# Optimization experiments

Hardware: AMD Instinct MI355X
Metric: run time of the kernel (lower is better)

The kernel has to match this reference:

```python
import jax, jax.numpy as jnp
import numpy as np

N = 100000
E = 1200000
D = 64  # g_dim == h2_dim, heads=1


def setup_inputs() -> dict:
    key = jax.random.key(0)
    ks = jax.random.split(key, 12)
    s = 1.0 / np.sqrt(D)
    node_features = jax.random.normal(ks[0], (N, D), dtype=jnp.float32)
    edge_index = jax.random.randint(ks[1], (2, E), 0, N, dtype=jnp.int64)
    edge_type = jax.random.randint(ks[2], (E,), 0, 4, dtype=jnp.int64)
    Wq = jax.random.uniform(ks[3], (D, D), jnp.float32, -s, s)
    bq = jax.random.uniform(ks[4], (D,), jnp.float32, -s, s)
    Wk = jax.random.uniform(ks[5], (D, D), jnp.float32, -s, s)
    bk = jax.random.uniform(ks[6], (D,), jnp.float32, -s, s)
    Wv = jax.random.uniform(ks[7], (D, D), jnp.float32, -s, s)
    bv = jax.random.uniform(ks[8], (D,), jnp.float32, -s, s)
    Wskip = jax.random.uniform(ks[9], (D, D), jnp.float32, -s, s)
    bskip = jax.random.uniform(ks[10], (D,), jnp.float32, -s, s)
    return dict(node_features=node_features, edge_index=edge_index,
                edge_type=edge_type, Wq=Wq, bq=bq, Wk=Wk, bk=bk,
                Wv=Wv, bv=bv, Wskip=Wskip, bskip=bskip)


def _transformer_conv(x, edge_index, Wq, bq, Wk, bk, Wv, bv, Wskip, bskip):
    src, dst = edge_index[0], edge_index[1]
    q = x @ Wq + bq          # [N, D] queries (for targets)
    k = x @ Wk + bk          # [N, D] keys (for sources)
    v = x @ Wv + bv          # [N, D] values (for sources)
    scale = 1.0 / jnp.sqrt(jnp.asarray(D, x.dtype))
    # per-edge attention logits: (q_dst . k_src) / sqrt(D)   [E]
    logits = jnp.sum(q[dst] * k[src], axis=-1) * scale
    # segment softmax over incoming edges of each destination node
    seg_max = jax.ops.segment_max(logits, dst, num_segments=N)
    seg_max = jnp.where(jnp.isfinite(seg_max), seg_max, 0.0)
    ex = jnp.exp(logits - seg_max[dst])
    seg_sum = jax.ops.segment_sum(ex, dst, num_segments=N)
    alpha = ex / (seg_sum[dst] + 1e-16)                      # [E]
    # attention-weighted scatter-aggregate of source values
    out = jax.ops.segment_sum(alpha[:, None] * v[src], dst, num_segments=N)
    # root/skip connection
    return out + x @ Wskip + bskip


def reference(node_features, edge_index, edge_type, Wq, bq, Wk, bk, Wv, bv, Wskip, bskip):
    # edge_type is accepted but unused, matching the original forward.
    return _transformer_conv(node_features, edge_index, Wq, bq, Wk, bk, Wv, bv, Wskip, bskip)
```

## Files before the change

kernel.cpp:

```cpp
#include <hip/hip_runtime.h>
#include <hip/hip_fp16.h>

#define D 64
#define BSH 9
#define SPLIT_CH 4096
#define NH 512
#define QSCALE 0.18033688f

typedef _Float16 f16x2 __attribute__((ext_vector_type(2)));
typedef _Float16 f16x8 __attribute__((ext_vector_type(8)));
typedef float f32x4 __attribute__((ext_vector_type(4)));

__device__ __forceinline__ float fdot2f(f16x2 a, f16x2 b, float c) {
#if __has_builtin(__builtin_amdgcn_fdot2)
    return __builtin_amdgcn_fdot2(a, b, c, false);
#else
    return fmaf((float)a.x, (float)b.x, fmaf((float)a.y, (float)b.y, c));
#endif
}

__device__ __forceinline__ f16x2 shxor_h2(f16x2 v, int m) {
    int i = __builtin_bit_cast(int, v);
    i = __shfl_xor(i, m);
    return __builtin_bit_cast(f16x2, i);
}

__device__ __forceinline__ unsigned packh2(float a, float b) {
    __half2 h = __floats2half2_rn(a, b);
    return __builtin_bit_cast(unsigned, h);
}

__global__ __launch_bounds__(256) void k_prep(
    const float* __restrict__ Wq, const float* __restrict__ Wk,
    const float* __restrict__ Wv, const float* __restrict__ Wsk,
    const float* __restrict__ bq, const float* __restrict__ bk,
    const float* __restrict__ bv, const float* __restrict__ bsk,
    const int* __restrict__ ei, unsigned* __restrict__ wpk,
    float* __restrict__ ball, int* __restrict__ ghist, int e_cnt)
{
    const int t = threadIdx.x;
    if (blockIdx.x < 32) {
        const int u    = blockIdx.x * 256 + t;
        const int i2   = u & 3;
        const int lane = (u >> 2) & 63;
        const int ks   = (u >> 8) & 1;
        const int mt   = u >> 9;
        const int ncol = mt * 16 + (lane & 15);
        const int k0   = ks * 32 + ((lane >> 4) << 3) + (i2 << 1);
        const float* W; int c; float sc = 1.f;
        if      (ncol <  64) { W = Wq;  c = ncol;       sc = QSCALE; }
        else if (ncol < 128) { W = Wk;  c = ncol - 64;  }
        else if (ncol < 192) { W = Wv;  c = ncol - 128; }
        else                 { W = Wsk; c = ncol - 192; }
        wpk[u] = packh2(W[k0 * 64 + c] * sc, W[(k0 + 1) * 64 + c] * sc);
    } else if (blockIdx.x == 32) {
        float b;
        if      (t <  64) b = bq[t] * QSCALE;
        else if (t < 128) b = bk[t - 64];
        else if (t < 192) b = bv[t - 128];
        else              b = bsk[t - 192];
        ball[t] = b;
    } else {
        __shared__ int h[256];
        h[t] = 0;
        __syncthreads();
        const int hb    = blockIdx.x - 33;
        const int chunk = (e_cnt + NH - 1) / NH;
        const int c0    = hb * chunk;
        const int c1    = min(c0 + chunk, e_cnt);
        for (int i = c0 + t; i < c1; i += 256)
            atomicAdd(&h[ei[e_cnt + i] >> BSH], 1);
        __syncthreads();
        if (h[t]) atomicAdd(&ghist[t], h[t]);
    }
}

__global__ __launch_bounds__(256) void k_linsplit(
    const float* __restrict__ x, const unsigned* __restrict__ wpk,
    const float* __restrict__ ball, const int* __restrict__ ei,
    const int* __restrict__ ghist, int* __restrict__ gcur0,
    unsigned* __restrict__ qh, unsigned* __restrict__ kvh,
    float* __restrict__ out, unsigned* __restrict__ epack,
    int n, int e_cnt, int NLIN)
{
    __shared__ __align__(16) union {
        struct {
            unsigned vals[SPLIT_CH];
            unsigned char bkt[SPLIT_CH];
            int hist[256], start[256], cur[256], base[256], s2[256], sg[256];
        } sp;
        _Float16 xsh[16][72];
    } sm;
    const int t = threadIdx.x;

    if (blockIdx.x >= NLIN) {
        unsigned* vals = sm.sp.vals;
        unsigned char* bkt = sm.sp.bkt;
        int* hist  = sm.sp.hist;
        int* start = sm.sp.start;
        int* cur   = sm.sp.cur;
        int* base  = sm.sp.base;
        int* s2    = sm.sp.s2;
        int* sg    = sm.sp.sg;

        const int e0  = (blockIdx.x - NLIN) * SPLIT_CH;
        const int cnt = min(SPLIT_CH, e_cnt - e0);

        hist[t] = 0;
        __syncthreads();
        for (int i = t; i < cnt; i += 256)
            atomicAdd(&hist[ei[e_cnt + e0 + i] >> BSH], 1);
        __syncthreads();

        {
            const int v = hist[t];
            const int g = ghist[t];
            s2[t] = v;
            sg[t] = g;
            __syncthreads();
            for (int off = 1; off < 256; off <<= 1) {
                const int a1 = (t >= off) ? s2[t - off] : 0;
                const int a2 = (t >= off) ? sg[t - off] : 0;
                __syncthreads();
                s2[t] += a1;
                sg[t] += a2;
                __syncthreads();
            }
            start[t] = s2[t] - v;
            cur[t]   = s2[t] - v;
            base[t]  = v ? (sg[t] - g + atomicAdd(&gcur0[t], v)) : 0;
        }
        __syncthreads();

        for (int i = t; i < cnt; i += 256) {
            const int s = ei[e0 + i];
            const int d = ei[e_cnt + e0 + i];
            const int b = d >> BSH;
            const int r = atomicAdd(&cur[b], 1);
            vals[r] = ((unsigned)s << BSH) | (unsigned)(d & 511);
            bkt[r]  = (unsigned char)b;
        }
        __syncthreads();

        for (int i = t; i < cnt; i += 256) {
            const int b = bkt[i];
            epack[base[b] + (i - start[b])] = vals[i];
        }
        return;
    }

    const int node0 = blockIdx.x * 16;
    {
        const float4* xg = (const float4*)(x + (size_t)node0 * 64);
        const int row = t >> 4, c4 = (t & 15) << 2;
        if (node0 + row < n) {
            const float4 v = xg[t];
            f16x2* dst = (f16x2*)&sm.xsh[row][c4];
            dst[0] = f16x2{(_Float16)v.x, (_Float16)v.y};
            dst[1] = f16x2{(_Float16)v.z, (_Float16)v.w};
        }
    }
    __syncthreads();

    const int w  = t >> 6;
    const int l  = t & 63;
    const int nd = l & 15;
    const int kg = l >> 4;

    f32x4 acc0 = {0.f, 0.f, 0.f, 0.f};
    f32x4 acc1 = acc0, acc2 = acc0, acc3 = acc0;
    const uint4* wpk4 = (const uint4*)wpk;

#pragma unroll
    for (int ks = 0; ks < 2; ++ks) {
        const f16x8 bfrag = *(const f16x8*)&sm.xsh[nd][ks * 32 + kg * 8];
        const int fb = (w * 4 * 2 + ks) * 64 + l;
        const f16x8 a0 = __builtin_bit_cast(f16x8, wpk4[fb]);
        const f16x8 a1 = __builtin_bit_cast(f16x8, wpk4[fb + 128]);
        const f16x8 a2 = __builtin_bit_cast(f16x8, wpk4[fb + 256]);
        const f16x8 a3 = __builtin_bit_cast(f16x8, wpk4[fb + 384]);
        acc0 = __builtin_amdgcn_mfma_f32_16x16x32_f16(a0, bfrag, acc0, 0, 0, 0);
        acc1 = __builtin_amdgcn_mfma_f32_16x16x32_f16(a1, bfrag, acc1, 0, 0, 0);
        acc2 = __builtin_amdgcn_mfma_f32_16x16x32_f16(a2, bfrag, acc2, 0, 0, 0);
        acc3 = __builtin_amdgcn_mfma_f32_16x16x32_f16(a3, bfrag, acc3, 0, 0, 0);
    }

    const int node = node0 + nd;
    if (node >= n) return;

    f32x4 accs[4] = {acc0, acc1, acc2, acc3};
#pragma unroll
    for (int m4 = 0; m4 < 4; ++m4) {
        const int gc = (w * 4 + m4) * 16 + kg * 4;
        const float4 bb = ((const float4*)ball)[gc >> 2];
        const float v0 = accs[m4][0] + bb.x;
        const float v1 = accs[m4][1] + bb.y;
        const float v2 = accs[m4][2] + bb.z;
        const float v3 = accs[m4][3] + bb.w;
        if (w == 3) {
            ((float4*)out)[(size_t)node * 16 + ((gc - 192) >> 2)] =
                make_float4(v0, v1, v2, v3);
        } else {
            uint2 u;
            u.x = packh2(v0, v1);
            u.y = packh2(v2, v3);
            if (w == 0)
                ((uint2*)qh)[(size_t)node * 16 + (gc >> 2)] = u;
            else if (w == 1)
                ((uint2*)kvh)[(size_t)node * 32 + ((gc - 64) >> 2)] = u;
            else
                ((uint2*)kvh)[(size_t)node * 32 + 16 + ((gc - 128) >> 2)] = u;
        }
    }
}

__global__ __launch_bounds__(512) void k_nodesort(
    const unsigned* __restrict__ epack, const int* __restrict__ ghist,
    int* __restrict__ esrc, int* __restrict__ endoff, int n)
{
    __shared__ int h[512], cur[512], s[512];
    __shared__ int sbase;
    const int b = blockIdx.x;
    const int t = threadIdx.x;

    s[t] = (t < 256) ? ghist[t] : 0;
    __syncthreads();
    for (int off = 1; off < 512; off <<= 1) {
        const int add = (t >= off) ? s[t - off] : 0;
        __syncthreads();
        s[t] += add;
        __syncthreads();
    }
    if (t == 0) sbase = (b == 0) ? 0 : s[b - 1];
    __syncthreads();
    const int base = sbase;
    const int cnt  = ghist[b];

    h[t] = 0;
    __syncthreads();
    for (int i = t; i < cnt; i += 512)
        atomicAdd(&h[epack[base + i] & 511], 1);
    __syncthreads();

    const int v = h[t];
    s[t] = v;
    __syncthreads();
    for (int off = 1; off < 512; off <<= 1) {
        const int add = (t >= off) ? s[t - off] : 0;
        __syncthreads();
        s[t] += add;
        __syncthreads();
    }
    cur[t] = s[t] - v;
    const int node = (b << BSH) + t;
    if (node < n) endoff[node] = base + s[t];
    __syncthreads();

    for (int i = t; i < cnt; i += 512) {
        const unsigned p = epack[base + i];
        const int r = atomicAdd(&cur[p & 511], 1);
        esrc[base + r] = (int)(p >> BSH);
    }
}

__global__ __launch_bounds__(256) void k_attn(
    const uint4* __restrict__ qh4, const uint4* __restrict__ kv4,
    const int* __restrict__ endoff, const int* __restrict__ esrc,
    float* __restrict__ out, int n)
{
    const int t = threadIdx.x;
    const int node = blockIdx.x * 4 + (t >> 6);
    if (node >= n) return;
    const int lane = t & 63;
    const int g = lane >> 3;
    const int l = lane & 7;

    const int beg = (node == 0) ? 0 : endoff[node - 1];
    const int end = endoff[node];
    const int last = end - 1;

    float4 o0 = make_float4(0.f, 0.f, 0.f, 0.f);
    float4 o1 = o0;
    if (g == 0) {
        o0 = ((const float4*)out)[(size_t)node * 16 + 2 * l];
        o1 = ((const float4*)out)[(size_t)node * 16 + 2 * l + 1];
    }

    const uint4 qu = qh4[(size_t)node * 8 + l];
    const f16x2* qp = (const f16x2*)&qu;

    f16x2 a0 = {(_Float16)0.f, (_Float16)0.f};
    f16x2 a1 = a0, a2 = a0, a3 = a0;
    float den = 0.f;

    int b2 = beg;
    for (; end - b2 > 8; b2 += 16) {
        const int iA = b2 + 2 * g;
        const int iB = iA + 1;
        const int sA = esrc[min(iA, last)];
        const int sB = esrc[min(iB, last)];
        const uint4 kuA = kv4[(size_t)sA * 16 + l];
        const uint4 vuA = kv4[(size_t)sA * 16 + 8 + l];
        const uint4 kuB = kv4[(size_t)sB * 16 + l];
        const uint4 vuB = kv4[(size_t)sB * 16 + 8 + l];
        const f16x2* kpA = (const f16x2*)&kuA;
        const f16x2* vpA = (const f16x2*)&vuA;
        const f16x2* kpB = (const f16x2*)&kuB;
        const f16x2* vpB = (const f16x2*)&vuB;

        float dA = fdot2f(qp[0], kpA[0], 0.f);
        float dB = fdot2f(qp[0], kpB[0], 0.f);
        dA = fdot2f(qp[1], kpA[1], dA);
        dB = fdot2f(qp[1], kpB[1], dB);
        dA = fdot2f(qp[2], kpA[2], dA);
        dB = fdot2f(qp[2], kpB[2], dB);
        dA = fdot2f(qp[3], kpA[3], dA);
        dB = fdot2f(qp[3], kpB[3], dB);
        dA += __shfl_xor(dA, 1);  dB += __shfl_xor(dB, 1);
        dA += __shfl_xor(dA, 2);  dB += __shfl_xor(dB, 2);
        dA += __shfl_xor(dA, 4);  dB += __shfl_xor(dB, 4);

        const float eA = (iA < end) ? exp2f(dA) : 0.f;
        const float eB = (iB < end) ? exp2f(dB) : 0.f;
        den += eA + eB;
        const _Float16 ehA = (_Float16)eA;
        const _Float16 ehB = (_Float16)eB;
        const f16x2 e2A = {ehA, ehA};
        const f16x2 e2B = {ehB, ehB};
        a0 += e2A * vpA[0];  a0 += e2B * vpB[0];
        a1 += e2A * vpA[1];  a1 += e2B * vpB[1];
        a2 += e2A * vpA[2];  a2 += e2B * vpB[2];
        a3 += e2A * vpA[3];  a3 += e2B * vpB[3];
    }
    for (; b2 < end; b2 += 8) {
        const int i = b2 + g;
        const int s = esrc[min(i, last)];
        const uint4 ku = kv4[(size_t)s * 16 + l];
        const uint4 vu = kv4[(size_t)s * 16 + 8 + l];
        const f16x2* kp = (const f16x2*)&ku;
        const f16x2* vp = (const f16x2*)&vu;

        float d = fdot2f(qp[0], kp[0], 0.f);
        d = fdot2f(qp[1], kp[1], d);
        d = fdot2f(qp[2], kp[2], d);
        d = fdot2f(qp[3], kp[3], d);
        d += __shfl_xor(d, 1);
        d += __shfl_xor(d, 2);
        d += __shfl_xor(d, 4);

        const float e = (i < end) ? exp2f(d) : 0.f;
        den += e;
        const _Float16 eh = (_Float16)e;
        const f16x2 e2 = {eh, eh};
        a0 += e2 * vp[0];
        a1 += e2 * vp[1];
        a2 += e2 * vp[2];
        a3 += e2 * vp[3];
    }

#pragma unroll
    for (int m = 8; m <= 32; m <<= 1) {
        den += __shfl_xor(den, m);
        a0 += shxor_h2(a0, m);
        a1 += shxor_h2(a1, m);
        a2 += shxor_h2(a2, m);
        a3 += shxor_h2(a3, m);
    }

    if (g == 0) {
        const float inv = 1.f / (den + 1e-16f);
        float4 r0, r1;
        r0.x = o0.x + (float)a0.x * inv;
        r0.y = o0.y + (float)a0.y * inv;
        r0.z = o0.z + (float)a1.x * inv;
        r0.w = o0.w + (float)a1.y * inv;
        r1.x = o1.x + (float)a2.x * inv;
        r1.y = o1.y + (float)a2.y * inv;
        r1.z = o1.z + (float)a3.x * inv;
        r1.w = o1.w + (float)a3.y * inv;
        ((float4*)out)[(size_t)node * 16 + 2 * l]     = r0;
        ((float4*)out)[(size_t)node * 16 + 2 * l + 1] = r1;
    }
}

extern "C" void kernel_launch(void* const* d_in, const int* in_sizes, int n_in,
                              void* d_out, int out_size, void* d_ws, size_t ws_size,
                              hipStream_t stream)
{
    const float* x   = (const float*)d_in[0];
    const int*   ei  = (const int*)d_in[1];
    const float* Wq  = (const float*)d_in[3];
    const float* bq  = (const float*)d_in[4];
    const float* Wk  = (const float*)d_in[5];
    const float* bk  = (const float*)d_in[6];
    const float* Wv  = (const float*)d_in[7];
    const float* bv  = (const float*)d_in[8];
    const float* Wsk = (const float*)d_in[9];
    const float* bsk = (const float*)d_in[10];
    float* out = (float*)d_out;

    const int n      = in_sizes[0] / D;
    const int e_cnt  = in_sizes[1] / 2;
    const int nbkt   = (n + 511) >> BSH;
    const int NLIN   = (n + 15) / 16;
    const int NSPLIT = (e_cnt + SPLIT_CH - 1) / SPLIT_CH;

    unsigned* qh     = (unsigned*)d_ws;
    unsigned* kvh    = qh + (size_t)n * 32;
    int*      esrc   = (int*)(kvh + (size_t)n * 64);
    unsigned* epack  = (unsigned*)(esrc + e_cnt);
    int*      endoff = (int*)(epack + e_cnt);
    int*      ghist  = endoff + n;
    int*      gcur0  = ghist + 256;
    float*    ball   = (float*)(gcur0 + 256);
    unsigned* wpk    = (unsigned*)(ball + 256);

    hipMemsetAsync(ghist, 0, 512 * sizeof(int), stream);

    k_prep<<<33 + NH, 256, 0, stream>>>(
        Wq, Wk, Wv, Wsk, bq, bk, bv, bsk, ei, wpk, ball, ghist, e_cnt);

    k_linsplit<<<NLIN + NSPLIT, 256, 0, stream>>>(
        x, wpk, ball, ei, ghist, gcur0, qh, kvh, out, epack, n, e_cnt, NLIN);

    k_nodesort<<<nbkt, 512, 0, stream>>>(
        epack, ghist, esrc, endoff, n);

    k_attn<<<(n + 3) / 4, 256, 0, stream>>>(
        (const uint4*)qh, (const uint4*)kvh, endoff, esrc, out, n);
}
```

Baseline: 124.1 us.

## Co-schedule projection GEMM with node sort instead of with edge split

The edge bucket-split now runs as its own kernel with smaller chunks (1024 edges per block), and the per-node counting sort is fused into the linear-projection kernel, which uses 512-thread blocks covering 32 nodes. The goal is to overlap the dense projection with the heavier node-sort stage and to shrink the split kernel's shared-memory footprint for better occupancy. In exchange there are more split blocks, each doing a global atomic per bucket, and the projection blocks now share a launch shape with the sort blocks. The number of kernel launches stays the same.

New measurement: 136.4 us. +9.9%, slower.

```diff
diff --git a/kernel.cpp b/kernel.cpp
--- a/kernel.cpp
+++ b/kernel.cpp
@@ -3,7 +3,7 @@
 
 #define D 64
 #define BSH 9
-#define SPLIT_CH 4096
+#define SPLIT_CH 1024
 #define NH 512
 #define QSCALE 0.18033688f
 
@@ -75,85 +75,126 @@
     }
 }
 
-__global__ __launch_bounds__(256) void k_linsplit(
+__global__ __launch_bounds__(256) void k_split(
+    const int* __restrict__ ei, const int* __restrict__ ghist,
+    int* __restrict__ gcur0, unsigned* __restrict__ epack, int e_cnt)
+{
+    __shared__ unsigned vals[SPLIT_CH];
+    __shared__ unsigned char bkt[SPLIT_CH];
+    __shared__ int hist[256], start[256], cur[256], base[256], s2[256], sg[256];
+
+    const int t  = threadIdx.x;
+    const int e0 = blockIdx.x * SPLIT_CH;
+    const int cnt = min(SPLIT_CH, e_cnt - e0);
+
+    hist[t] = 0;
+    __syncthreads();
+    for (int i = t; i < cnt; i += 256)
+        atomicAdd(&hist[ei[e_cnt + e0 + i] >> BSH], 1);
+    __syncthreads();
+
+    {
+        const int v = hist[t];
+        const int g = ghist[t];
+        s2[t] = v;
+        sg[t] = g;
+        __syncthreads();
+        for (int off = 1; off < 256; off <<= 1) {
+            const int a1 = (t >= off) ? s2[t - off] : 0;
+            const int a2 = (t >= off) ? sg[t - off] : 0;
+            __syncthreads();
+            s2[t] += a1;
+            sg[t] += a2;
+            __syncthreads();
+        }
+        start[t] = s2[t] - v;
+        cur[t]   = s2[t] - v;
+        base[t]  = v ? (sg[t] - g + atomicAdd(&gcur0[t], v)) : 0;
+    }
+    __syncthreads();
+
+    for (int i = t; i < cnt; i += 256) {
+        const int s = ei[e0 + i];
+        const int d = ei[e_cnt + e0 + i];
+        const int b = d >> BSH;
+        const int r = atomicAdd(&cur[b], 1);
+        vals[r] = ((unsigned)s << BSH) | (unsigned)(d & 511);
+        bkt[r]  = (unsigned char)b;
+    }
+    __syncthreads();
+
+    for (int i = t; i < cnt; i += 256) {
+        const int b = bkt[i];
+        epack[base[b] + (i - start[b])] = vals[i];
+    }
+}
+
+__global__ __launch_bounds__(512) void k_linsort(
     const float* __restrict__ x, const unsigned* __restrict__ wpk,
-    const float* __restrict__ ball, const int* __restrict__ ei,
-    const int* __restrict__ ghist, int* __restrict__ gcur0,
+    const float* __restrict__ ball,
+    const unsigned* __restrict__ epack, const int* __restrict__ ghist,
     unsigned* __restrict__ qh, unsigned* __restrict__ kvh,
-    float* __restrict__ out, unsigned* __restrict__ epack,
-    int n, int e_cnt, int NLIN)
+    float* __restrict__ out, int* __restrict__ esrc,
+    int* __restrict__ endoff, int n, int NLIN)
 {
-    __shared__ __align__(16) union {
-        struct {
-            unsigned vals[SPLIT_CH];
-            unsigned char bkt[SPLIT_CH];
-            int hist[256], start[256], cur[256], base[256], s2[256], sg[256];
-        } sp;
-        _Float16 xsh[16][72];
+    __shared__ union {
+        struct { int s[512]; int h[512]; int cur[512]; int sbase; } ns;
+        __align__(16) _Float16 xsh[32][72];
     } sm;
     const int t = threadIdx.x;
 
     if (blockIdx.x >= NLIN) {
-        unsigned* vals = sm.sp.vals;
-        unsigned char* bkt = sm.sp.bkt;
-        int* hist  = sm.sp.hist;
-        int* start = sm.sp.start;
-        int* cur   = sm.sp.cur;
-        int* base  = sm.sp.base;
-        int* s2    = sm.sp.s2;
-        int* sg    = sm.sp.sg;
-
-        const int e0  = (blockIdx.x - NLIN) * SPLIT_CH;
-        const int cnt = min(SPLIT_CH, e_cnt - e0);
-
-        hist[t] = 0;
-        __syncthreads();
-        for (int i = t; i < cnt; i += 256)
-            atomicAdd(&hist[ei[e_cnt + e0 + i] >> BSH], 1);
-        __syncthreads();
-
-        {
-            const int v = hist[t];
-            const int g = ghist[t];
-            s2[t] = v;
-            sg[t] = g;
-            __syncthreads();
-            for (int off = 1; off < 256; off <<= 1) {
-                const int a1 = (t >= off) ? s2[t - off] : 0;
-                const int a2 = (t >= off) ? sg[t - off] : 0;
-                __syncthreads();
-                s2[t] += a1;
-                sg[t] += a2;
-                __syncthreads();
-            }
-            start[t] = s2[t] - v;
-            cur[t]   = s2[t] - v;
-            base[t]  = v ? (sg[t] - g + atomicAdd(&gcur0[t], v)) : 0;
-        }
-        __syncthreads();
-
-        for (int i = t; i < cnt; i += 256) {
-            const int s = ei[e0 + i];
-            const int d = ei[e_cnt + e0 + i];
-            const int b = d >> BSH;
-            const int r = atomicAdd(&cur[b], 1);
-            vals[r] = ((unsigned)s << BSH) | (unsigned)(d & 511);
-            bkt[r]  = (unsigned char)b;
-        }
-        __syncthreads();
-
-        for (int i = t; i < cnt; i += 256) {
-            const int b = bkt[i];
-            epack[base[b] + (i - start[b])] = vals[i];
+        int* s   = sm.ns.s;
+        int* h   = sm.ns.h;
+        int* cur = sm.ns.cur;
+        const int b = blockIdx.x - NLIN;
+
+        s[t] = (t < 256) ? ghist[t] : 0;
+        __syncthreads();
+        for (int off = 1; off < 512; off <<= 1) {
+            const int add = (t >= off) ? s[t - off] : 0;
+            __syncthreads();
+            s[t] += add;
+            __syncthreads();
+        }
+        if (t == 0) sm.ns.sbase = (b == 0) ? 0 : s[b - 1];
+        __syncthreads();
+        const int base = sm.ns.sbase;
+        const int cnt  = ghist[b];
+
+        h[t] = 0;
+        __syncthreads();
+        for (int i = t; i < cnt; i += 512)
+            atomicAdd(&h[epack[base + i] & 511], 1);
+        __syncthreads();
+
+        const int v = h[t];
+        s[t] = v;
+        __syncthreads();
+        for (int off = 1; off < 512; off <<= 1) {
+            const int add = (t >= off) ? s[t - off] : 0;
+            __syncthreads();
+            s[t] += add;
+            __syncthreads();
+        }
+        cur[t] = s[t] - v;
+        const int node = (b << BSH) + t;
+        if (node < n) endoff[node] = base + s[t];
+        __syncthreads();
+
+        for (int i = t; i < cnt; i += 512) {
+            const unsigned p = epack[base + i];
+            const int r = atomicAdd(&cur[p & 511], 1);
+            esrc[base + r] = (int)(p >> BSH);
         }
         return;
     }
 
-    const int node0 = blockIdx.x * 16;
+    const int row0 = blockIdx.x * 32;
     {
-        const float4* xg = (const float4*)(x + (size_t)node0 * 64);
+        const float4* xg = (const float4*)(x + (size_t)row0 * 64);
         const int row = t >> 4, c4 = (t & 15) << 2;
-        if (node0 + row < n) {
+        if (row0 + row < n) {
             const float4 v = xg[t];
             f16x2* dst = (f16x2*)&sm.xsh[row][c4];
             dst[0] = f16x2{(_Float16)v.x, (_Float16)v.y};
@@ -162,10 +203,12 @@
     }
     __syncthreads();
 
-    const int w  = t >> 6;
-    const int l  = t & 63;
-    const int nd = l & 15;
-    const int kg = l >> 4;
+    const int w     = t >> 6;
+    const int tile  = w >> 2;
+    const int wrole = w & 3;
+    const int l     = t & 63;
+    const int nd    = l & 15;
+    const int kg    = l >> 4;
 
     f32x4 acc0 = {0.f, 0.f, 0.f, 0.f};
     f32x4 acc1 = acc0, acc2 = acc0, acc3 = acc0;
@@ -173,8 +216,8 @@
 
 #pragma unroll
     for (int ks = 0; ks < 2; ++ks) {
-        const f16x8 bfrag = *(const f16x8*)&sm.xsh[nd][ks * 32 + kg * 8];
-        const int fb = (w * 4 * 2 + ks) * 64 + l;
+        const f16x8 bfrag = *(const f16x8*)&sm.xsh[tile * 16 + nd][ks * 32 + kg * 8];
+        const int fb = (wrole * 4 * 2 + ks) * 64 + l;
         const f16x8 a0 = __builtin_bit_cast(f16x8, wpk4[fb]);
         const f16x8 a1 = __builtin_bit_cast(f16x8, wpk4[fb + 128]);
         const f16x8 a2 = __builtin_bit_cast(f16x8, wpk4[fb + 256]);
@@ -185,81 +228,32 @@
         acc3 = __builtin_amdgcn_mfma_f32_16x16x32_f16(a3, bfrag, acc3, 0, 0, 0);
     }
 
-    const int node = node0 + nd;
+    const int node = row0 + tile * 16 + nd;
     if (node >= n) return;
 
     f32x4 accs[4] = {acc0, acc1, acc2, acc3};
 #pragma unroll
     for (int m4 = 0; m4 < 4; ++m4) {
-        const int gc = (w * 4 + m4) * 16 + kg * 4;
+        const int gc = (wrole * 4 + m4) * 16 + kg * 4;
         const float4 bb = ((const float4*)ball)[gc >> 2];
         const float v0 = accs[m4][0] + bb.x;
         const float v1 = accs[m4][1] + bb.y;
         const float v2 = accs[m4][2] + bb.z;
         const float v3 = accs[m4][3] + bb.w;
-        if (w == 3) {
+        if (wrole == 3) {
             ((float4*)out)[(size_t)node * 16 + ((gc - 192) >> 2)] =
                 make_float4(v0, v1, v2, v3);
         } else {
             uint2 u;
             u.x = packh2(v0, v1);
             u.y = packh2(v2, v3);
-            if (w == 0)
+            if (wrole == 0)
                 ((uint2*)qh)[(size_t)node * 16 + (gc >> 2)] = u;
-            else if (w == 1)
+            else if (wrole == 1)
                 ((uint2*)kvh)[(size_t)node * 32 + ((gc - 64) >> 2)] = u;
             else
                 ((uint2*)kvh)[(size_t)node * 32 + 16 + ((gc - 128) >> 2)] = u;
         }
-    }
-}
-
-__global__ __launch_bounds__(512) void k_nodesort(
-    const unsigned* __restrict__ epack, const int* __restrict__ ghist,
-    int* __restrict__ esrc, int* __restrict__ endoff, int n)
-{
-    __shared__ int h[512], cur[512], s[512];
-    __shared__ int sbase;
-    const int b = blockIdx.x;
-    const int t = threadIdx.x;
-
-    s[t] = (t < 256) ? ghist[t] : 0;
-    __syncthreads();
-    for (int off = 1; off < 512; off <<= 1) {
-        const int add = (t >= off) ? s[t - off] : 0;
-        __syncthreads();
-        s[t] += add;
-        __syncthreads();
-    }
-    if (t == 0) sbase = (b == 0) ? 0 : s[b - 1];
-    __syncthreads();
-    const int base = sbase;
-    const int cnt  = ghist[b];
-
-    h[t] = 0;
-    __syncthreads();
-    for (int i = t; i < cnt; i += 512)
-        atomicAdd(&h[epack[base + i] & 511], 1);
-    __syncthreads();
-
-    const int v = h[t];
-    s[t] = v;
-    __syncthreads();
-    for (int off = 1; off < 512; off <<= 1) {
-        const int add = (t >= off) ? s[t - off] : 0;
-        __syncthreads();
-        s[t] += add;
-        __syncthreads();
-    }
-    cur[t] = s[t] - v;
-    const int node = (b << BSH) + t;
-    if (node < n) endoff[node] = base + s[t];
-    __syncthreads();
-
-    for (int i = t; i < cnt; i += 512) {
-        const unsigned p = epack[base + i];
-        const int r = atomicAdd(&cur[p & 511], 1);
-        esrc[base + r] = (int)(p >> BSH);
     }
 }
 
@@ -402,7 +396,7 @@
     const int n      = in_sizes[0] / D;
     const int e_cnt  = in_sizes[1] / 2;
     const int nbkt   = (n + 511) >> BSH;
-    const int NLIN   = (n + 15) / 16;
+    const int NLIN   = (n + 31) / 32;
     const int NSPLIT = (e_cnt + SPLIT_CH - 1) / SPLIT_CH;
 
     unsigned* qh     = (unsigned*)d_ws;
@@ -420,11 +414,10 @@
     k_prep<<<33 + NH, 256, 0, stream>>>(
         Wq, Wk, Wv, Wsk, bq, bk, bv, bsk, ei, wpk, ball, ghist, e_cnt);
 
-    k_linsplit<<<NLIN + NSPLIT, 256, 0, stream>>>(
-        x, wpk, ball, ei, ghist, gcur0, qh, kvh, out, epack, n, e_cnt, NLIN);
-
-    k_nodesort<<<nbkt, 512, 0, stream>>>(
-        epack, ghist, esrc, endoff, n);
+    k_split<<<NSPLIT, 256, 0, stream>>>(ei, ghist, gcur0, epack, e_cnt);
+
+    k_linsort<<<NLIN + nbkt, 512, 0, stream>>>(
+        x, wpk, ball, epack, ghist, qh, kvh, out, esrc, endoff, n, NLIN);
 
     k_attn<<<(n + 3) / 4, 256, 0, stream>>>(
         (const uint4*)qh, (const uint4*)kvh, endoff, esrc, out, n);
```
